# Optimization experiments

Hardware: AMD Instinct MI355X
Metric: run time of the kernel (lower is better)

## Reference

```python
import jax, jax.numpy as jnp
import numpy as np

EMBED_DIM = 1024
NUM_HEADS = 16
HEAD_DIM = EMBED_DIM // NUM_HEADS


def setup_inputs() -> dict:
    key = jax.random.key(0)
    ks = jax.random.split(key, 12)
    B, S, E = 2, 2048, EMBED_DIM
    scale = 1.0 / np.sqrt(E)
    inp = {
        "query": jax.random.normal(ks[0], (B, S, E), dtype=jnp.float32),
        "key": jax.random.normal(ks[1], (B, S, E), dtype=jnp.float32),
        "value": jax.random.normal(ks[2], (B, S, E), dtype=jnp.float32),
        "key_padding_mask": jax.random.randint(ks[3], (B, S), 0, 2).astype(bool),
        # Linear params (torch nn.Linear: y = x @ W.T + b)
        "Wq": jax.random.normal(ks[4], (E, E), dtype=jnp.float32) * scale,
        "bq": jnp.zeros((E,), dtype=jnp.float32),
        "Wk": jax.random.normal(ks[5], (E, E), dtype=jnp.float32) * scale,
        "bk": jnp.zeros((E,), dtype=jnp.float32),
        "Wv": jax.random.normal(ks[6], (E, E), dtype=jnp.float32) * scale,
        "bv": jnp.zeros((E,), dtype=jnp.float32),
        "Wo": jax.random.normal(ks[7], (E, E), dtype=jnp.float32) * scale,
        "bo": jnp.zeros((E,), dtype=jnp.float32),
    }
    return inp


def reference(query, key, value, key_padding_mask, Wq, bq, Wk, bk, Wv, bv, Wo, bo):
    B, Sq, E = query.shape
    H, D = NUM_HEADS, HEAD_DIM

    def split_heads(x, W, b):
        y = x @ W.T + b                      # [B, S, E]
        return y.reshape(B, -1, H, D).transpose(0, 2, 1, 3)  # [B, H, S, D]

    q = split_heads(query, Wq, bq)
    k = split_heads(key, Wk, bk)
    v = split_heads(value, Wv, bv)

    scores = jnp.einsum("bhqd,bhkd->bhqk", q, k) / jnp.sqrt(jnp.float32(D))
    scores = jnp.where(key_padding_mask[:, None, None, :], -jnp.inf, scores)
    probs = jax.nn.softmax(scores, axis=-1)  # dropout p=0.0 -> identity
    attn = jnp.einsum("bhqk,bhkd->bhqd", probs, v)
    attn = attn.transpose(0, 2, 1, 3).reshape(B, Sq, E)
    return attn @ Wo.T + bo
```

## Files before the change

### kernel.cpp

```cpp
#include <hip/hip_runtime.h>
#include <hip/hip_bf16.h>

#define BATCH 2
#define SEQ   2048
#define EMBED 1024
#define NHEAD 16
#define HDIM  64

typedef __bf16 bf16x8 __attribute__((ext_vector_type(8)));
typedef float  floatx4 __attribute__((ext_vector_type(4)));

__global__ void detect_kernel(const void* qptr, const void* mptr, int* flags) {
    if (threadIdx.x != 0 || blockIdx.x != 0) return;
    const unsigned short* u = (const unsigned short*)qptr;
    int sane = 0;
    for (int i = 0; i < 64; ++i) {
        int e = (u[2 * i] >> 7) & 0xff;
        if (e >= 117 && e <= 137) sane++;
    }
    flags[0] = (sane >= 40) ? 1 : 0;
    const unsigned int* w = (const unsigned int*)mptr;
    int all01 = 1, allf = 1;
    for (int i = 0; i < 64; ++i) {
        unsigned int x = w[i];
        if (!(x == 0u || x == 1u)) all01 = 0;
        if (!(x == 0u || x == 0x3F800000u)) allf = 0;
    }
    flags[1] = (all01 || allf) ? 0 : 1;
}

__global__ void mask_bits(const void* mptr, const int* flags,
                          unsigned long long* mb) {
    const int i = blockIdx.x * 64 + threadIdx.x;
    int v;
    if (flags[1]) v = (((const unsigned char*)mptr)[i] != 0);
    else          v = (((const unsigned int*)mptr)[i] != 0u);
    unsigned long long bal = __ballot(v);
    if (threadIdx.x == 0) mb[blockIdx.x] = bal;
}

struct ConvAll { const void* src[7]; void* dst[7]; unsigned n[7]; };

__global__ __launch_bounds__(256) void convert_all(ConvAll a, const int* flags) {
    if (flags[0]) return;
    const int t = blockIdx.y;
    const unsigned n8 = a.n[t] / 8;
    const unsigned stride = gridDim.x * blockDim.x;
    for (unsigned i = blockIdx.x * blockDim.x + threadIdx.x; i < n8; i += stride) {
        const unsigned base = i * 8;
        const float* s = (const float*)a.src[t] + base;
        __hip_bfloat16 tmp[8];
#pragma unroll
        for (int j = 0; j < 8; ++j) tmp[j] = __float2bfloat16(s[j]);
        *(uint4*)((__hip_bfloat16*)a.dst[t] + base) = *(const uint4*)tmp;
    }
}

__device__ __forceinline__ void gload_lds16(const __hip_bfloat16* g, __bf16* l) {
    __builtin_amdgcn_global_load_lds(
        (const __attribute__((address_space(1))) unsigned int*)g,
        (__attribute__((address_space(3))) unsigned int*)l, 16, 0, 0);
}

struct GemmIO {
    const void* Xr; const __hip_bfloat16* Xc;
    const void* Wr; const __hip_bfloat16* Wc;
    const void* br;
    void* Y;
};
struct GemmArgs { GemmIO io[3]; };

__global__ __launch_bounds__(256, 2) void gemm_mfma(
        GemmArgs args, int M, int N, int K, const int* flags, int omode) {
    const GemmIO io = args.io[blockIdx.z];
    const int isbf = flags[0];
    const __hip_bfloat16* Xp = isbf ? (const __hip_bfloat16*)io.Xr : io.Xc;
    const __hip_bfloat16* Wp = isbf ? (const __hip_bfloat16*)io.Wr : io.Wc;
    __shared__ __bf16 Xs[128 * 64];
    __shared__ __bf16 Ws[128 * 64];
    const int lane = threadIdx.x & 63, wv = threadIdx.x >> 6;
    const int wr = wv >> 1, wc = wv & 1;
    const int l = lane & 15, quad = lane >> 4;
    const int row0 = blockIdx.y * 128, col0 = blockIdx.x * 128;

    const int srow = lane >> 3;
    const int schunk = (lane & 7) ^ srow;
    const __hip_bfloat16* xbase = Xp + (size_t)(row0 + srow) * K + schunk * 8;
    const __hip_bfloat16* wbase = Wp + (size_t)(col0 + srow) * K + schunk * 8;

    floatx4 acc[4][4] = {};

    for (int k0 = 0; k0 < K; k0 += 64) {
        __syncthreads();
#pragma unroll
        for (int i = 0; i < 4; ++i) {
            const int instr = wv * 4 + i;
            gload_lds16(xbase + (size_t)instr * 8 * K + k0, &Xs[instr * 512]);
        }
#pragma unroll
        for (int i = 0; i < 4; ++i) {
            const int instr = wv * 4 + i;
            gload_lds16(wbase + (size_t)instr * 8 * K + k0, &Ws[instr * 512]);
        }
        __syncthreads();
#pragma unroll
        for (int kk = 0; kk < 2; ++kk) {
            bf16x8 af[4], bfr[4];
#pragma unroll
            for (int m = 0; m < 4; ++m)
                af[m] = *(const bf16x8*)
                    &Xs[(wr * 64 + m * 16 + l) * 64 + ((kk * 4 + quad) ^ (l & 7)) * 8];
#pragma unroll
            for (int n = 0; n < 4; ++n)
                bfr[n] = *(const bf16x8*)
                    &Ws[(wc * 64 + n * 16 + l) * 64 + ((kk * 4 + quad) ^ (l & 7)) * 8];
#pragma unroll
            for (int m = 0; m < 4; ++m)
#pragma unroll
                for (int n = 0; n < 4; ++n)
                    acc[m][n] = __builtin_amdgcn_mfma_f32_16x16x32_bf16(
                        af[m], bfr[n], acc[m][n], 0, 0, 0);
        }
    }

#pragma unroll
    for (int m = 0; m < 4; ++m) {
#pragma unroll
        for (int n = 0; n < 4; ++n) {
            const int col = col0 + wc * 64 + n * 16 + l;
            const float bv = isbf
                ? __bfloat162float(((const __hip_bfloat16*)io.br)[col])
                : ((const float*)io.br)[col];
#pragma unroll
            for (int r = 0; r < 4; ++r) {
                const int row = row0 + wr * 64 + m * 16 + quad * 4 + r;
                const float v = acc[m][n][r] + bv;
                if (omode == 0 || isbf)
                    ((__hip_bfloat16*)io.Y)[(size_t)row * N + col] = __float2bfloat16(v);
                else
                    ((float*)io.Y)[(size_t)row * N + col] = v;
            }
        }
    }
}

__global__ __launch_bounds__(256) void transpose_v(
        const __hip_bfloat16* __restrict__ Vp, __hip_bfloat16* __restrict__ Vt) {
    __shared__ __bf16 Ts[64][72];
    const int bh = blockIdx.x, b = bh >> 4, h = bh & 15;
    const int s0 = blockIdx.y * 64;
    const int t = threadIdx.x;
    const int s = t >> 2, c = t & 3;
#pragma unroll
    for (int half = 0; half < 2; ++half) {
        const int cc = c + half * 4;
        bf16x8 v = *(const bf16x8*)(Vp + (size_t)(b * SEQ + s0 + s) * EMBED +
                                    h * HDIM + cc * 8);
#pragma unroll
        for (int j = 0; j < 8; ++j) Ts[cc * 8 + j][s] = v[j];
    }
    __syncthreads();
    const int d = t >> 2;
#pragma unroll
    for (int half = 0; half < 2; ++half) {
        const int cc = c + half * 4;
        bf16x8 v = *(const bf16x8*)&Ts[d][cc * 8];
        *(bf16x8*)(Vt + ((size_t)bh * HDIM + d) * SEQ + s0 + cc * 8) = v;
    }
}

__global__ __launch_bounds__(256) void attn_mfma(
        const __hip_bfloat16* __restrict__ Qb,
        const __hip_bfloat16* __restrict__ Kb,
        const __hip_bfloat16* __restrict__ Vt,
        const unsigned long long* __restrict__ mbits,
        __hip_bfloat16* __restrict__ Ao) {
    const int bh = blockIdx.x, b = bh >> 4, h = bh & 15;
    const int q0 = blockIdx.y * 128;
    const int wv = threadIdx.x >> 6, lane = threadIdx.x & 63;
    const int l = lane & 15, quad = lane >> 4;

    __shared__ __bf16 Ks[128 * 64];
    __shared__ __bf16 Vs[64 * 128];

    bf16x8 aQ[2][2];
#pragma unroll
    for (int g = 0; g < 2; ++g) {
        const int qrow = q0 + wv * 32 + g * 16 + l;
        const __hip_bfloat16* qp =
            Qb + ((size_t)(b * SEQ + qrow)) * EMBED + h * HDIM + quad * 8;
        aQ[g][0] = *(const bf16x8*)qp;
        aQ[g][1] = *(const bf16x8*)(qp + 32);
    }

    floatx4 O[2][4] = {};
    floatx4 Ol[2] = {};
    const float SC2 = 0.125f * 1.44269504088896f;
    const int rho = 8 * (l >> 2) + (l & 3);

    bf16x8 vone;
#pragma unroll
    for (int j = 0; j < 8; ++j) vone[j] = (__bf16)1.0f;

    const int ksrow = lane >> 3, kpc = lane & 7;
    const int vsrow = lane >> 4, vpc = lane & 15;

    for (int k0 = 0; k0 < SEQ; k0 += 128) {
        __syncthreads();
#pragma unroll
        for (int i = 0; i < 4; ++i) {
            const int row = wv * 32 + i * 8 + ksrow;
            const int sc = kpc ^ ((row & 3) | (((row >> 3) & 1) << 2));
            gload_lds16(Kb + ((size_t)(b * SEQ + k0 + row)) * EMBED + h * HDIM +
                            sc * 8,
                        &Ks[(wv * 32 + i * 8) * 64]);
        }
#pragma unroll
        for (int i = 0; i < 4; ++i) {
            const int row = wv * 16 + i * 4 + vsrow;
            const int sc = vpc ^ (row & 15);
            gload_lds16(Vt + ((size_t)(bh * HDIM + row)) * SEQ + k0 + sc * 8,
                        &Vs[(wv * 16 + i * 4) * 128]);
        }
        __syncthreads();

        const unsigned long long mw0 = mbits[b * 32 + (k0 >> 6)];
        const unsigned long long mw1 = mbits[b * 32 + (k0 >> 6) + 1];

#pragma unroll
        for (int kh2 = 0; kh2 < 2; ++kh2) {
            bf16x8 a0[4], a1[4];
#pragma unroll
            for (int n = 0; n < 4; ++n) {
                const int rr = kh2 * 64 + 32 * (n >> 1) + 4 * (n & 1) + rho;
                const int f = (rr & 3) | (((rr >> 3) & 1) << 2);
                a0[n] = *(const bf16x8*)&Ks[rr * 64 + ((quad) ^ f) * 8];
                a1[n] = *(const bf16x8*)&Ks[rr * 64 + ((quad + 4) ^ f) * 8];
            }
            bf16x8 bv[2][4];
#pragma unroll
            for (int kh = 0; kh < 2; ++kh)
#pragma unroll
                for (int dt = 0; dt < 4; ++dt) {
                    const int c = kh2 * 8 + kh * 4 + quad;
                    bv[kh][dt] =
                        *(const bf16x8*)&Vs[(dt * 16 + l) * 128 + (c ^ l) * 8];
                }
            const unsigned long long mw = kh2 ? mw1 : mw0;
            const unsigned mb0 = (unsigned)(mw >> (8 * quad)) & 0xffu;
            const unsigned mb1 = (unsigned)(mw >> (32 + 8 * quad)) & 0xffu;

#pragma unroll
            for (int g = 0; g < 2; ++g) {
                floatx4 S[4];
#pragma unroll
                for (int n = 0; n < 4; ++n) {
                    floatx4 c = {};
                    c = __builtin_amdgcn_mfma_f32_16x16x32_bf16(a0[n], aQ[g][0],
                                                                c, 0, 0, 0);
                    c = __builtin_amdgcn_mfma_f32_16x16x32_bf16(a1[n], aQ[g][1],
                                                                c, 0, 0, 0);
                    S[n] = c;
                }
#pragma unroll
                for (int n = 0; n < 4; ++n) {
                    const unsigned byt = (n < 2) ? mb0 : mb1;
#pragma unroll
                    for (int r = 0; r < 4; ++r) {
                        const float p = exp2f(S[n][r] * SC2);
                        S[n][r] = ((byt >> (4 * (n & 1) + r)) & 1u) ? 0.f : p;
                    }
                }
#pragma unroll
                for (int kh = 0; kh < 2; ++kh) {
                    bf16x8 ap;
#pragma unroll
                    for (int j = 0; j < 4; ++j) {
                        ap[j]     = (__bf16)S[2 * kh][j];
                        ap[j + 4] = (__bf16)S[2 * kh + 1][j];
                    }
#pragma unroll
                    for (int dt = 0; dt < 4; ++dt)
                        O[g][dt] = __builtin_amdgcn_mfma_f32_16x16x32_bf16(
                            ap, bv[kh][dt], O[g][dt], 0, 0, 0);
                    Ol[g] = __builtin_amdgcn_mfma_f32_16x16x32_bf16(
                        ap, vone, Ol[g], 0, 0, 0);
                }
            }
        }
    }
#pragma unroll
    for (int g = 0; g < 2; ++g)
#pragma unroll
        for (int r = 0; r < 4; ++r) {
            const float lr = Ol[g][r];
            const float inv = (lr > 0.f) ? (1.f / lr) : 0.f;
            const int row = q0 + wv * 32 + g * 16 + quad * 4 + r;
#pragma unroll
            for (int dt = 0; dt < 4; ++dt)
                Ao[((size_t)(b * SEQ + row)) * EMBED + h * HDIM + dt * 16 + l] =
                    __float2bfloat16(O[g][dt][r] * inv);
        }
}

extern "C" void kernel_launch(void* const* d_in, const int* in_sizes, int n_in,
                              void* d_out, int out_size, void* d_ws, size_t ws_size,
                              hipStream_t stream) {
    const void* query = d_in[0];
    const void* key   = d_in[1];
    const void* value = d_in[2];
    const void* mask  = d_in[3];

    char* ws = (char*)d_ws;
    int* flags = (int*)ws;
    unsigned long long* mbits = (unsigned long long*)(ws + 1024);
    const size_t TEN = (size_t)BATCH * SEQ * EMBED;
    const size_t WEL = (size_t)EMBED * EMBED;
    char* p = ws + 32768;
    __hip_bfloat16* Qc  = (__hip_bfloat16*)p;  p += TEN * 2;
    __hip_bfloat16* Kc  = (__hip_bfloat16*)p;  p += TEN * 2;
    __hip_bfloat16* Vc  = (__hip_bfloat16*)p;  p += TEN * 2;
    __hip_bfloat16* Wqc = (__hip_bfloat16*)p;  p += WEL * 2;
    __hip_bfloat16* Wkc = (__hip_bfloat16*)p;  p += WEL * 2;
    __hip_bfloat16* Wvc = (__hip_bfloat16*)p;  p += WEL * 2;
    __hip_bfloat16* Woc = (__hip_bfloat16*)p;  p += WEL * 2;
    __hip_bfloat16* Qb  = (__hip_bfloat16*)p;  p += TEN * 2;
    __hip_bfloat16* Kb  = (__hip_bfloat16*)p;  p += TEN * 2;
    __hip_bfloat16* Vp  = (__hip_bfloat16*)p;  p += TEN * 2;
    __hip_bfloat16* Ao  = Qc;
    __hip_bfloat16* Vt  = Kc;

    const int M = BATCH * SEQ;

    detect_kernel<<<1, 64, 0, stream>>>(query, mask, flags);

    ConvAll ca;
    ca.src[0] = query;    ca.dst[0] = Qc;  ca.n[0] = (unsigned)TEN;
    ca.src[1] = key;      ca.dst[1] = Kc;  ca.n[1] = (unsigned)TEN;
    ca.src[2] = value;    ca.dst[2] = Vc;  ca.n[2] = (unsigned)TEN;
    ca.src[3] = d_in[4];  ca.dst[3] = Wqc; ca.n[3] = (unsigned)WEL;
    ca.src[4] = d_in[6];  ca.dst[4] = Wkc; ca.n[4] = (unsigned)WEL;
    ca.src[5] = d_in[8];  ca.dst[5] = Wvc; ca.n[5] = (unsigned)WEL;
    ca.src[6] = d_in[10]; ca.dst[6] = Woc; ca.n[6] = (unsigned)WEL;
    convert_all<<<dim3(256, 7), 256, 0, stream>>>(ca, flags);

    mask_bits<<<BATCH * SEQ / 64, 64, 0, stream>>>(mask, flags, mbits);

    GemmArgs qkv;
    qkv.io[0] = { query, Qc, d_in[4],  Wqc, d_in[5],  (void*)Qb };
    qkv.io[1] = { key,   Kc, d_in[6],  Wkc, d_in[7],  (void*)Kb };
    qkv.io[2] = { value, Vc, d_in[8],  Wvc, d_in[9],  (void*)Vp };
    gemm_mfma<<<dim3(EMBED / 128, M / 128, 3), 256, 0, stream>>>(
        qkv, M, EMBED, EMBED, flags, 0);

    transpose_v<<<dim3(BATCH * NHEAD, SEQ / 64), 256, 0, stream>>>(Vp, Vt);

    attn_mfma<<<dim3(BATCH * NHEAD, SEQ / 128), 256, 0, stream>>>(Qb, Kb, Vt,
                                                                  mbits, Ao);

    GemmArgs og;
    og.io[0] = { Ao, Ao, d_in[10], Woc, d_in[11], d_out };
    og.io[1] = og.io[0];
    og.io[2] = og.io[0];
    gemm_mfma<<<dim3(EMBED / 128, M / 128, 1), 256, 0, stream>>>(
        og, M, EMBED, EMBED, flags, 1);
}
```

Measured before the change: 263.4 us.

## Split attention over two key halves with merge kernel; fold softmax scale into Q

The attention kernel now splits the key range in two along a new grid dimension, so it launches twice as many blocks (1024 instead of 512). A new merge kernel combines the two unnormalised partial outputs using the stored row sums. The softmax scale and log2e factor are folded into the Q projection epilogue, which removes a multiply per score. Detect and mask-bit kernels are fused into one launch, and convert_all uses fewer blocks. The split adds an extra round-trip of two bf16 partial tensors plus a merge pass, and partial outputs are rounded to bf16 before merging. Without max-subtraction, unnormalised partials could be larger and lose precision.

Result: slower. 276.5 us (+5.0%).

```diff
diff --git a/kernel.cpp b/kernel.cpp
--- a/kernel.cpp
+++ b/kernel.cpp
@@ -10,15 +10,8 @@
 typedef __bf16 bf16x8 __attribute__((ext_vector_type(8)));
 typedef float  floatx4 __attribute__((ext_vector_type(4)));
 
-__global__ void detect_kernel(const void* qptr, const void* mptr, int* flags) {
-    if (threadIdx.x != 0 || blockIdx.x != 0) return;
-    const unsigned short* u = (const unsigned short*)qptr;
-    int sane = 0;
-    for (int i = 0; i < 64; ++i) {
-        int e = (u[2 * i] >> 7) & 0xff;
-        if (e >= 117 && e <= 137) sane++;
-    }
-    flags[0] = (sane >= 40) ? 1 : 0;
+__global__ void mask_flags_bits(const void* qptr, const void* mptr,
+                                unsigned long long* mb, int* flags) {
     const unsigned int* w = (const unsigned int*)mptr;
     int all01 = 1, allf = 1;
     for (int i = 0; i < 64; ++i) {
@@ -26,17 +19,23 @@
         if (!(x == 0u || x == 1u)) all01 = 0;
         if (!(x == 0u || x == 0x3F800000u)) allf = 0;
     }
-    flags[1] = (all01 || allf) ? 0 : 1;
-}
-
-__global__ void mask_bits(const void* mptr, const int* flags,
-                          unsigned long long* mb) {
+    const int bytemask = (all01 || allf) ? 0 : 1;
     const int i = blockIdx.x * 64 + threadIdx.x;
     int v;
-    if (flags[1]) v = (((const unsigned char*)mptr)[i] != 0);
+    if (bytemask) v = (((const unsigned char*)mptr)[i] != 0);
     else          v = (((const unsigned int*)mptr)[i] != 0u);
     unsigned long long bal = __ballot(v);
     if (threadIdx.x == 0) mb[blockIdx.x] = bal;
+    if (blockIdx.x == 0 && threadIdx.x == 0) {
+        const unsigned short* u = (const unsigned short*)qptr;
+        int sane = 0;
+        for (int k = 0; k < 64; ++k) {
+            int e = (u[2 * k] >> 7) & 0xff;
+            if (e >= 117 && e <= 137) sane++;
+        }
+        flags[0] = (sane >= 40) ? 1 : 0;
+        flags[1] = bytemask;
+    }
 }
 
 struct ConvAll { const void* src[7]; void* dst[7]; unsigned n[7]; };
@@ -67,6 +66,7 @@
     const void* Wr; const __hip_bfloat16* Wc;
     const void* br;
     void* Y;
+    float osc;
 };
 struct GemmArgs { GemmIO io[3]; };
 
@@ -134,7 +134,7 @@
 #pragma unroll
             for (int r = 0; r < 4; ++r) {
                 const int row = row0 + wr * 64 + m * 16 + quad * 4 + r;
-                const float v = acc[m][n][r] + bv;
+                const float v = (acc[m][n][r] + bv) * io.osc;
                 if (omode == 0 || isbf)
                     ((__hip_bfloat16*)io.Y)[(size_t)row * N + col] = __float2bfloat16(v);
                 else
@@ -174,9 +174,12 @@
         const __hip_bfloat16* __restrict__ Kb,
         const __hip_bfloat16* __restrict__ Vt,
         const unsigned long long* __restrict__ mbits,
-        __hip_bfloat16* __restrict__ Ao) {
+        __hip_bfloat16* __restrict__ O0p,
+        __hip_bfloat16* __restrict__ O1p,
+        float* __restrict__ Lp) {
     const int bh = blockIdx.x, b = bh >> 4, h = bh & 15;
     const int q0 = blockIdx.y * 128;
+    const int z = blockIdx.z;
     const int wv = threadIdx.x >> 6, lane = threadIdx.x & 63;
     const int l = lane & 15, quad = lane >> 4;
 
@@ -195,7 +198,6 @@
 
     floatx4 O[2][4] = {};
     floatx4 Ol[2] = {};
-    const float SC2 = 0.125f * 1.44269504088896f;
     const int rho = 8 * (l >> 2) + (l & 3);
 
     bf16x8 vone;
@@ -205,7 +207,8 @@
     const int ksrow = lane >> 3, kpc = lane & 7;
     const int vsrow = lane >> 4, vpc = lane & 15;
 
-    for (int k0 = 0; k0 < SEQ; k0 += 128) {
+    const int kbeg = z * (SEQ / 2), kend = kbeg + SEQ / 2;
+    for (int k0 = kbeg; k0 < kend; k0 += 128) {
         __syncthreads();
 #pragma unroll
         for (int i = 0; i < 4; ++i) {
@@ -267,7 +270,7 @@
                     const unsigned byt = (n < 2) ? mb0 : mb1;
 #pragma unroll
                     for (int r = 0; r < 4; ++r) {
-                        const float p = exp2f(S[n][r] * SC2);
+                        const float p = exp2f(S[n][r]);
                         S[n][r] = ((byt >> (4 * (n & 1) + r)) & 1u) ? 0.f : p;
                     }
                 }
@@ -289,18 +292,48 @@
             }
         }
     }
+    __hip_bfloat16* Op = z ? O1p : O0p;
 #pragma unroll
     for (int g = 0; g < 2; ++g)
 #pragma unroll
         for (int r = 0; r < 4; ++r) {
-            const float lr = Ol[g][r];
-            const float inv = (lr > 0.f) ? (1.f / lr) : 0.f;
             const int row = q0 + wv * 32 + g * 16 + quad * 4 + r;
 #pragma unroll
             for (int dt = 0; dt < 4; ++dt)
-                Ao[((size_t)(b * SEQ + row)) * EMBED + h * HDIM + dt * 16 + l] =
-                    __float2bfloat16(O[g][dt][r] * inv);
-        }
+                Op[((size_t)(b * SEQ + row)) * EMBED + h * HDIM + dt * 16 + l] =
+                    __float2bfloat16(O[g][dt][r]);
+            if (l == 0)
+                Lp[((size_t)z * NHEAD * BATCH + bh) * SEQ + row] = Ol[g][r];
+        }
+}
+
+__global__ __launch_bounds__(256) void merge_attn(
+        const __hip_bfloat16* __restrict__ O0p,
+        const __hip_bfloat16* __restrict__ O1p,
+        const float* __restrict__ Lp,
+        __hip_bfloat16* __restrict__ Ao) {
+    const unsigned TEN8 = (unsigned)(BATCH * SEQ * EMBED / 8);
+    const unsigned stride = gridDim.x * blockDim.x;
+    const unsigned ZSTRIDE = BATCH * NHEAD * SEQ;
+    for (unsigned i = blockIdx.x * blockDim.x + threadIdx.x; i < TEN8;
+         i += stride) {
+        const unsigned base = i * 8;
+        const unsigned row = base >> 10;
+        const unsigned h = (base >> 6) & 15;
+        const unsigned b = row >> 11;
+        const unsigned srow = row & 2047;
+        const unsigned bh = b * NHEAD + h;
+        const unsigned lidx = bh * SEQ + srow;
+        const float lsum = Lp[lidx] + Lp[ZSTRIDE + lidx];
+        const float inv = (lsum > 0.f) ? (1.f / lsum) : 0.f;
+        const bf16x8 v0 = *(const bf16x8*)(O0p + base);
+        const bf16x8 v1 = *(const bf16x8*)(O1p + base);
+        __hip_bfloat16 tmp[8];
+#pragma unroll
+        for (int j = 0; j < 8; ++j)
+            tmp[j] = __float2bfloat16(((float)v0[j] + (float)v1[j]) * inv);
+        *(uint4*)(Ao + base) = *(const uint4*)tmp;
+    }
 }
 
 extern "C" void kernel_launch(void* const* d_in, const int* in_sizes, int n_in,
@@ -329,10 +362,14 @@
     __hip_bfloat16* Vp  = (__hip_bfloat16*)p;  p += TEN * 2;
     __hip_bfloat16* Ao  = Qc;
     __hip_bfloat16* Vt  = Kc;
+    __hip_bfloat16* O0p = Vc;
+    __hip_bfloat16* O1p = Vp;
+    float* Lp = (float*)Wqc;
 
     const int M = BATCH * SEQ;
-
-    detect_kernel<<<1, 64, 0, stream>>>(query, mask, flags);
+    const float QSCALE = 0.125f * 1.44269504088896f;
+
+    mask_flags_bits<<<M / 64, 64, 0, stream>>>(query, mask, mbits, flags);
 
     ConvAll ca;
     ca.src[0] = query;    ca.dst[0] = Qc;  ca.n[0] = (unsigned)TEN;
@@ -342,24 +379,24 @@
     ca.src[4] = d_in[6];  ca.dst[4] = Wkc; ca.n[4] = (unsigned)WEL;
     ca.src[5] = d_in[8];  ca.dst[5] = Wvc; ca.n[5] = (unsigned)WEL;
     ca.src[6] = d_in[10]; ca.dst[6] = Woc; ca.n[6] = (unsigned)WEL;
-    convert_all<<<dim3(256, 7), 256, 0, stream>>>(ca, flags);
-
-    mask_bits<<<BATCH * SEQ / 64, 64, 0, stream>>>(mask, flags, mbits);
+    convert_all<<<dim3(64, 7), 256, 0, stream>>>(ca, flags);
 
     GemmArgs qkv;
-    qkv.io[0] = { query, Qc, d_in[4],  Wqc, d_in[5],  (void*)Qb };
-    qkv.io[1] = { key,   Kc, d_in[6],  Wkc, d_in[7],  (void*)Kb };
-    qkv.io[2] = { value, Vc, d_in[8],  Wvc, d_in[9],  (void*)Vp };
+    qkv.io[0] = { query, Qc, d_in[4],  Wqc, d_in[5],  (void*)Qb, QSCALE };
+    qkv.io[1] = { key,   Kc, d_in[6],  Wkc, d_in[7],  (void*)Kb, 1.0f };
+    qkv.io[2] = { value, Vc, d_in[8],  Wvc, d_in[9],  (void*)Vp, 1.0f };
     gemm_mfma<<<dim3(EMBED / 128, M / 128, 3), 256, 0, stream>>>(
         qkv, M, EMBED, EMBED, flags, 0);
 
     transpose_v<<<dim3(BATCH * NHEAD, SEQ / 64), 256, 0, stream>>>(Vp, Vt);
 
-    attn_mfma<<<dim3(BATCH * NHEAD, SEQ / 128), 256, 0, stream>>>(Qb, Kb, Vt,
-                                                                  mbits, Ao);
+    attn_mfma<<<dim3(BATCH * NHEAD, SEQ / 128, 2), 256, 0, stream>>>(
+        Qb, Kb, Vt, mbits, O0p, O1p, Lp);
+
+    merge_attn<<<1024, 256, 0, stream>>>(O0p, O1p, Lp, Ao);
 
     GemmArgs og;
-    og.io[0] = { Ao, Ao, d_in[10], Woc, d_in[11], d_out };
+    og.io[0] = { Ao, Ao, d_in[10], Woc, d_in[11], d_out, 1.0f };
     og.io[1] = og.io[0];
     og.io[2] = og.io[0];
     gemm_mfma<<<dim3(EMBED / 128, M / 128, 1), 256, 0, stream>>>(
```
